# Optimization experiments

Hardware: AMD Instinct MI355X
Metric: run time of the kernel (lower is better)

The kernel has to match this reference:

```python
import jax, jax.numpy as jnp
import numpy as np

B, T, E, H, K = 256, 512, 768, 100, 11
START, STOP = 9, 10
NEG = -1000.0


def setup_inputs() -> dict:
    key = jax.random.key(0)
    ks = jax.random.split(key, 12)
    s = 0.1
    Hd = H // 2  # per-direction hidden (bidirectional)
    trans = jax.random.normal(ks[9], (K, K), jnp.float32)
    trans = trans.at[:, START].set(NEG).at[STOP, :].set(NEG)
    return {
        "embeddings": jax.random.normal(ks[0], (B, T, E), jnp.float32),
        "input_mask": jnp.ones((B, T), jnp.int32),
        "W_ih_f": jax.random.normal(ks[1], (4 * Hd, E), jnp.float32) * s,
        "W_hh_f": jax.random.normal(ks[2], (4 * Hd, Hd), jnp.float32) * s,
        "b_f": jax.random.normal(ks[3], (4 * Hd,), jnp.float32) * s,
        "W_ih_b": jax.random.normal(ks[4], (4 * Hd, E), jnp.float32) * s,
        "W_hh_b": jax.random.normal(ks[5], (4 * Hd, Hd), jnp.float32) * s,
        "b_b": jax.random.normal(ks[6], (4 * Hd,), jnp.float32) * s,
        "W_out": jax.random.normal(ks[7], (K, H), jnp.float32) * s,
        "b_out": jax.random.normal(ks[8], (K,), jnp.float32) * s,
        "transitions": trans,
    }


def _lstm_dir(x, W_ih, W_hh, b, reverse):
    # x: [B, T, E] -> hidden states [B, T, Hd]; zero initial state.
    Bn = x.shape[0]
    Hd = W_hh.shape[1]

    def step(carry, xt):
        h, c = carry
        g = xt @ W_ih.T + h @ W_hh.T + b  # [B, 4*Hd], torch gate order i,f,g,o
        i, f, gg, o = jnp.split(g, 4, axis=-1)
        c = jax.nn.sigmoid(f) * c + jax.nn.sigmoid(i) * jnp.tanh(gg)
        h = jax.nn.sigmoid(o) * jnp.tanh(c)
        return (h, c), h

    init = (jnp.zeros((Bn, Hd), x.dtype), jnp.zeros((Bn, Hd), x.dtype))
    _, hs = jax.lax.scan(step, init, jnp.swapaxes(x, 0, 1), reverse=reverse)
    return jnp.swapaxes(hs, 0, 1)


def _emissions(embeddings, W_ih_f, W_hh_f, b_f, W_ih_b, W_hh_b, b_b, W_out, b_out):
    h_f = _lstm_dir(embeddings, W_ih_f, W_hh_f, b_f, reverse=False)
    h_b = _lstm_dir(embeddings, W_ih_b, W_hh_b, b_b, reverse=True)
    lstm_out = jnp.concatenate([h_f, h_b], axis=-1)  # [B, T, H]
    return lstm_out @ W_out.T + b_out  # [B, T, K]


def reference(embeddings, input_mask, W_ih_f, W_hh_f, b_f, W_ih_b, W_hh_b, b_b,
              W_out, b_out, transitions):
    logits = _emissions(embeddings, W_ih_f, W_hh_f, b_f, W_ih_b, W_hh_b, b_b,
                        W_out, b_out)  # [B, T, K]
    Bn = logits.shape[0]
    mask = (input_mask > 0)

    alpha0 = jnp.full((Bn, K), NEG, logits.dtype).at[:, START].set(0.0)
    idK = jnp.arange(K, dtype=jnp.int32)

    def step(alpha, inp):
        frame, m = inp  # frame [B,K], m [B] bool
        # smat[b, prev, cur] = alpha[b,prev] + frame[b,cur] + trans[prev,cur]
        smat = alpha[:, :, None] + frame[:, None, :] + transitions[None]
        bp = jnp.argmax(smat, axis=1).astype(jnp.int32)          # [B, K]
        new_alpha = jax.nn.logsumexp(smat, axis=1)               # [B, K]
        alpha = jnp.where(m[:, None], new_alpha, alpha)
        bp = jnp.where(m[:, None], bp, idK[None, :])
        return alpha, bp

    alpha_T, bps = jax.lax.scan(
        step, alpha0,
        (jnp.swapaxes(logits, 0, 1), jnp.swapaxes(mask, 0, 1)))  # bps [T,B,K]

    final = alpha_T + transitions[None, :, STOP]                 # [B, K]
    scores = jax.nn.logsumexp(final, axis=1)                     # [B]
    best = jnp.argmax(final, axis=1).astype(jnp.int32)           # [B]

    bidx = jnp.arange(Bn)

    def back(cur, bp_t):
        prev = bp_t[bidx, cur]
        return prev, prev

    # Original skips backtrace[0]; backtrack over positions 1..T-1.
    _, path_prefix = jax.lax.scan(back, best, bps[1:], reverse=True)  # [T-1, B]
    paths = jnp.concatenate(
        [jnp.swapaxes(path_prefix, 0, 1), best[:, None]], axis=1)     # [B, T]
    return scores, paths
```

## Files before the change

### kernel.cpp

```cpp
#include <hip/hip_runtime.h>
#include <math.h>


typedef _Float16 half8 __attribute__((ext_vector_type(8)));
typedef _Float16 half4 __attribute__((ext_vector_type(4)));
typedef float f32x4 __attribute__((ext_vector_type(4)));

__global__ __launch_bounds__(256) void k_gemm_split(
    const float* __restrict__ emb,
    const float* __restrict__ Wf,
    const float* __restrict__ Wb,
    float* __restrict__ xw)
{
    __shared__ _Float16 Ah[128 * 64];
    __shared__ _Float16 Al[128 * 64];
    __shared__ _Float16 Bh[80 * 64];
    __shared__ _Float16 Bl[80 * 64];

    const int bid = blockIdx.x;
    const int wg  = (bid & 7) * 640 + (bid >> 3);
    const int mt  = wg / 5;
    const int nb  = wg - mt * 5;
    const size_t m0 = (size_t)mt * 128;
    const int n0 = nb * 80;

    const int tid  = threadIdx.x;
    const int lane = tid & 63;
    const int w    = tid >> 6;
    const int grp  = lane >> 4;
    const int r16  = lane & 15;

    f32x4 acc[2][5];
    #pragma unroll
    for (int m = 0; m < 2; ++m)
        #pragma unroll
        for (int n = 0; n < 5; ++n) acc[m][n] = (f32x4){0.f, 0.f, 0.f, 0.f};

    for (int kt = 0; kt < 12; ++kt) {
        const int k0 = kt * 64;
        __syncthreads();

        #pragma unroll
        for (int j = 0; j < 8; ++j) {
            const int flat = j * 256 + tid;
            const int row  = flat >> 4;
            const int q    = flat & 15;
            const float4 v = *(const float4*)(emb + (m0 + row) * 768 + k0 + q * 4);
            half4 hv, lv;
            hv[0] = (_Float16)v.x; lv[0] = (_Float16)(v.x - (float)hv[0]);
            hv[1] = (_Float16)v.y; lv[1] = (_Float16)(v.y - (float)hv[1]);
            hv[2] = (_Float16)v.z; lv[2] = (_Float16)(v.z - (float)hv[2]);
            hv[3] = (_Float16)v.w; lv[3] = (_Float16)(v.w - (float)hv[3]);
            const int s    = (q >> 1) ^ (row & 7);
            const int addr = row * 64 + s * 8 + (q & 1) * 4;
            *(half4*)(Ah + addr) = hv;
            *(half4*)(Al + addr) = lv;
        }
        #pragma unroll
        for (int j = 0; j < 5; ++j) {
            const int flat = j * 256 + tid;
            const int row  = flat >> 4;
            const int q    = flat & 15;
            const int n    = n0 + row;
            const float* src = (n < 200) ? (Wf + (size_t)n * 768)
                                         : (Wb + (size_t)(n - 200) * 768);
            const float4 v = *(const float4*)(src + k0 + q * 4);
            half4 hv, lv;
            hv[0] = (_Float16)v.x; lv[0] = (_Float16)(v.x - (float)hv[0]);
            hv[1] = (_Float16)v.y; lv[1] = (_Float16)(v.y - (float)hv[1]);
            hv[2] = (_Float16)v.z; lv[2] = (_Float16)(v.z - (float)hv[2]);
            hv[3] = (_Float16)v.w; lv[3] = (_Float16)(v.w - (float)hv[3]);
            const int s    = (q >> 1) ^ (row & 7);
            const int addr = row * 64 + s * 8 + (q & 1) * 4;
            *(half4*)(Bh + addr) = hv;
            *(half4*)(Bl + addr) = lv;
        }
        __syncthreads();

        #pragma unroll
        for (int ks = 0; ks < 2; ++ks) {
            const int kslot = ks * 4 + grp;
            half8 ah[2], al[2], bh[5], bl[5];
            #pragma unroll
            for (int m = 0; m < 2; ++m) {
                const int row = w * 32 + m * 16 + r16;
                const int ad  = row * 64 + (kslot ^ (row & 7)) * 8;
                ah[m] = *(half8*)(Ah + ad);
                al[m] = *(half8*)(Al + ad);
            }
            #pragma unroll
            for (int n = 0; n < 5; ++n) {
                const int row = n * 16 + r16;
                const int ad  = row * 64 + (kslot ^ (row & 7)) * 8;
                bh[n] = *(half8*)(Bh + ad);
                bl[n] = *(half8*)(Bl + ad);
            }
            #pragma unroll
            for (int m = 0; m < 2; ++m)
                #pragma unroll
                for (int n = 0; n < 5; ++n) {
                    acc[m][n] = __builtin_amdgcn_mfma_f32_16x16x32_f16(ah[m], bh[n], acc[m][n], 0, 0, 0);
                    acc[m][n] = __builtin_amdgcn_mfma_f32_16x16x32_f16(ah[m], bl[n], acc[m][n], 0, 0, 0);
                    acc[m][n] = __builtin_amdgcn_mfma_f32_16x16x32_f16(al[m], bh[n], acc[m][n], 0, 0, 0);
                }
        }
    }

    #pragma unroll
    for (int m = 0; m < 2; ++m) {
        #pragma unroll
        for (int n = 0; n < 5; ++n) {
            #pragma unroll
            for (int i = 0; i < 4; ++i) {
                const size_t row = m0 + w * 32 + m * 16 + (lane >> 4) * 4 + i;
                const int    col = n0 + n * 16 + (lane & 15);
                xw[row * 400 + col] = acc[m][n][i];
            }
        }
    }
}

__global__ __launch_bounds__(256) void k_lstm(
    const float* __restrict__ xw,
    const float* __restrict__ Whh_f,
    const float* __restrict__ Whh_b,
    const float* __restrict__ bf_,
    const float* __restrict__ bb_,
    float* __restrict__ hout)
{
    const int b   = blockIdx.x >> 1;
    const int dir = blockIdx.x & 1;
    const int g   = threadIdx.x;

    __shared__ float h_s[52];
    __shared__ float g_s[200];

    const float* Whh  = dir ? Whh_b : Whh_f;
    const float* bias = dir ? bb_ : bf_;

    float w[52];
    float bg = 0.f;
    if (g < 200) {
        #pragma unroll
        for (int j = 0; j < 50; ++j) w[j] = Whh[g * 50 + j];
        w[50] = 0.f; w[51] = 0.f;
        bg = bias[g];
    } else {
        #pragma unroll
        for (int j = 0; j < 52; ++j) w[j] = 0.f;
    }

    if (g < 52) h_s[g] = 0.f;
    float c = 0.f;
    __syncthreads();

    const size_t base = (size_t)b * 512;

    float xv = 0.f;
    {
        int t0 = dir ? 511 : 0;
        if (g < 200) xv = xw[(base + t0) * 400 + dir * 200 + g];
    }

    for (int it = 0; it < 512; ++it) {
        const int t = dir ? (511 - it) : it;
        float xcur = xv;
        if (it + 1 < 512) {
            int tn = dir ? (510 - it) : (it + 1);
            if (g < 200) xv = xw[(base + tn) * 400 + dir * 200 + g];
        }

        float sum = bg + xcur;
        const float4* h4 = (const float4*)h_s;
        #pragma unroll
        for (int q = 0; q < 13; ++q) {
            float4 hv = h4[q];
            sum = fmaf(w[q * 4 + 0], hv.x, sum);
            sum = fmaf(w[q * 4 + 1], hv.y, sum);
            sum = fmaf(w[q * 4 + 2], hv.z, sum);
            sum = fmaf(w[q * 4 + 3], hv.w, sum);
        }
        if (g < 200) g_s[g] = sum;
        __syncthreads();

        if (g < 50) {
            float gi = g_s[g];
            float gf = g_s[g + 50];
            float gg = g_s[g + 100];
            float go = g_s[g + 150];
            float si = 1.f / (1.f + expf(-gi));
            float sf = 1.f / (1.f + expf(-gf));
            float so = 1.f / (1.f + expf(-go));
            c = sf * c + si * tanhf(gg);
            float h = so * tanhf(c);
            hout[(base + t) * 100 + dir * 50 + g] = h;
            h_s[g] = h;
        }
        __syncthreads();
    }
}

__global__ __launch_bounds__(256) void k_emis(
    const float* __restrict__ hout,
    const float* __restrict__ Wout,
    const float* __restrict__ bout,
    float* __restrict__ logits)
{
    __shared__ float Wl[1104];
    __shared__ float bl[11];
    const int tid = threadIdx.x;
    for (int i = tid; i < 1100; i += 256) Wl[i] = Wout[i];
    if (tid < 11) bl[tid] = bout[tid];
    __syncthreads();

    const size_t bt = (size_t)blockIdx.x * 256 + tid;
    const float4* h4 = (const float4*)(hout + bt * 100);
    float acc[11];
    #pragma unroll
    for (int k = 0; k < 11; ++k) acc[k] = bl[k];
    #pragma unroll
    for (int q = 0; q < 25; ++q) {
        float4 v = h4[q];
        #pragma unroll
        for (int k = 0; k < 11; ++k) {
            const float4 wv = *(const float4*)&Wl[k * 100 + q * 4];
            acc[k] = fmaf(v.x, wv.x, fmaf(v.y, wv.y, fmaf(v.z, wv.z, fmaf(v.w, wv.w, acc[k]))));
        }
    }
    #pragma unroll
    for (int k = 0; k < 11; ++k) logits[bt * 11 + k] = acc[k];
}

__global__ __launch_bounds__(64, 1) void k_crf(
    const float* __restrict__ logits,
    const int* __restrict__ mask,
    const float* __restrict__ trans,
    float* __restrict__ scores,
    float* __restrict__ paths)
{
    const int b = blockIdx.x;
    const int lane = threadIdx.x;

    __shared__ float smat[11 * 12];
    __shared__ float emat[11 * 12];
    __shared__ unsigned char bp[512][12];

    const int  pA = lane / 11, cA = lane - pA * 11;
    const bool hasB = (lane < 57);
    const int  iB = hasB ? (lane + 64) : 0;
    const int  pB = iB / 11, cB = iB - pB * 11;

    const float trA = trans[pA * 11 + cA];
    const float trB = hasB ? trans[pB * 11 + cB] : 0.f;

    float al_c = (lane == 9) ? 0.f : -1000.f;

    const size_t lbase = (size_t)b * 512;

    float fA = logits[lbase * 11 + cA];
    float fB = hasB ? logits[lbase * 11 + cB] : 0.f;
    int   m_cur = mask[lbase];

    for (int t = 0; t < 512; ++t) {
        float fA_n = 0.f, fB_n = 0.f; int m_n = 1;
        if (t + 1 < 512) {
            fA_n = logits[(lbase + t + 1) * 11 + cA];
            if (hasB) fB_n = logits[(lbase + t + 1) * 11 + cB];
            m_n = mask[lbase + t + 1];
        }

        const float alA = __shfl(al_c, pA);
        const float alB = __shfl(al_c, pB);
        const float vvA = (alA + fA) + trA;
        const float vvB = (alB + fB) + trB;
        smat[cA * 12 + pA] = vvA;
        if (hasB) smat[cB * 12 + pB] = vvB;

        float vmax = -1e30f; int amax = 0;
        if (lane < 11) {
            float v[11];
            #pragma unroll
            for (int p = 0; p < 11; ++p) v[p] = smat[lane * 12 + p];
            #pragma unroll
            for (int p = 0; p < 11; ++p) {
                if (v[p] > vmax) { vmax = v[p]; amax = p; }
            }
        }
        const float vmA = __shfl(vmax, cA);
        const float vmB = __shfl(vmax, cB);

        const float eA = expf(vvA - vmA);
        const float eB = expf(vvB - vmB);
        emat[cA * 12 + pA] = eA;
        if (hasB) emat[cB * 12 + pB] = eB;

        if (lane < 11) {
            float e[11];
            #pragma unroll
            for (int p = 0; p < 11; ++p) e[p] = emat[lane * 12 + p];
            float s = 0.f;
            #pragma unroll
            for (int p = 0; p < 11; ++p) s += e[p];
            const float na = vmax + logf(s);
            if (m_cur > 0) {
                al_c = na;
                bp[t][lane] = (unsigned char)amax;
            } else {
                bp[t][lane] = (unsigned char)lane;
            }
        }
        fA = fA_n; fB = fB_n; m_cur = m_n;
    }

    float fin = (lane < 11) ? (al_c + trans[lane * 11 + 10]) : -1e30f;
    float m = fin;
    int am = (lane < 11) ? lane : 1000;
    #pragma unroll
    for (int off = 8; off >= 1; off >>= 1) {
        float om = __shfl_xor(m, off, 16);
        int   oa = __shfl_xor(am, off, 16);
        if (om > m || (om == m && oa < am)) { m = om; am = oa; }
    }
    float s = (lane < 11) ? expf(fin - m) : 0.f;
    #pragma unroll
    for (int off = 8; off >= 1; off >>= 1) s += __shfl_xor(s, off, 16);

    if (lane == 0) {
        scores[b] = m + logf(s);
        int cur = am;
        paths[lbase + 511] = (float)cur;
        for (int t = 511; t >= 1; --t) {
            cur = bp[t][cur];
            paths[lbase + t - 1] = (float)cur;
        }
    }
}

extern "C" void kernel_launch(void* const* d_in, const int* in_sizes, int n_in,
                              void* d_out, int out_size, void* d_ws, size_t ws_size,
                              hipStream_t stream) {
    const float* emb   = (const float*)d_in[0];
    const int*   imask = (const int*)d_in[1];
    const float* Wihf  = (const float*)d_in[2];
    const float* Whhf  = (const float*)d_in[3];
    const float* bf_   = (const float*)d_in[4];
    const float* Wihb  = (const float*)d_in[5];
    const float* Whhb  = (const float*)d_in[6];
    const float* bb_   = (const float*)d_in[7];
    const float* Wout  = (const float*)d_in[8];
    const float* bout  = (const float*)d_in[9];
    const float* trans = (const float*)d_in[10];

    float* out = (float*)d_out;
    float* ws  = (float*)d_ws;
    float* xw     = ws;
    float* hout   = xw + (size_t)131072 * 400;
    float* logits = hout + (size_t)131072 * 100;

    k_gemm_split<<<5120, 256, 0, stream>>>(emb, Wihf, Wihb, xw);
    k_lstm<<<512, 256, 0, stream>>>(xw, Whhf, Whhb, bf_, bb_, hout);
    k_emis<<<512, 256, 0, stream>>>(hout, Wout, bout, logits);
    k_crf<<<256, 64, 0, stream>>>(logits, imask, trans, out, out + 256);
}
```

Before: 1.083 ms.

## Batch 16 sequences per LSTM block and compute recurrence with split-fp16 MFMA

The recurrent LSTM kernel now processes 16 batch chains per block (32 blocks total instead of 512). It computes h@W_hh^T each step with 16x16x32 f16 MFMA, splitting fp32 into hi/lo halves to keep near-fp32 accuracy. Weights are held as MFMA fragments in registers, and the input projection is double-buffered in shared memory. The gate math uses fast exp/rcp intrinsics and only one barrier per step. This targets the per-step latency and the low arithmetic density of one block per sequence. The cost is far fewer blocks on a large GPU, some approximation error from the fast intrinsics and split-fp16, and more shared-memory traffic.

```diff
diff --git a/kernel.cpp b/kernel.cpp
--- a/kernel.cpp
+++ b/kernel.cpp
@@ -120,7 +120,7 @@
     }
 }
 
-__global__ __launch_bounds__(256) void k_lstm(
+__global__ __launch_bounds__(256, 1) void k_lstm(
     const float* __restrict__ xw,
     const float* __restrict__ Whh_f,
     const float* __restrict__ Whh_b,
@@ -128,75 +128,141 @@
     const float* __restrict__ bb_,
     float* __restrict__ hout)
 {
-    const int b   = blockIdx.x >> 1;
-    const int dir = blockIdx.x & 1;
-    const int g   = threadIdx.x;
-
-    __shared__ float h_s[52];
-    __shared__ float g_s[200];
+    const int dir = blockIdx.x >> 4;
+    const int bc  = blockIdx.x & 15;
+    const int tid = threadIdx.x;
+    const int wv  = tid >> 6;
+    const int lane = tid & 63;
+    const int grp  = lane >> 4;
+    const int r16  = lane & 15;
+
+    __shared__ _Float16 Bh[208 * 64];
+    __shared__ _Float16 Bl[208 * 64];
+    __shared__ _Float16 Ahh[16 * 64];
+    __shared__ _Float16 Ahl[16 * 64];
+    __shared__ float g_s[16 * 208];
+    __shared__ float x_s[2][16 * 256];
+    __shared__ float bias_s[208];
 
     const float* Whh  = dir ? Whh_b : Whh_f;
     const float* bias = dir ? bb_ : bf_;
 
-    float w[52];
-    float bg = 0.f;
-    if (g < 200) {
-        #pragma unroll
-        for (int j = 0; j < 50; ++j) w[j] = Whh[g * 50 + j];
-        w[50] = 0.f; w[51] = 0.f;
-        bg = bias[g];
-    } else {
-        #pragma unroll
-        for (int j = 0; j < 52; ++j) w[j] = 0.f;
-    }
-
-    if (g < 52) h_s[g] = 0.f;
-    float c = 0.f;
+    for (int i = tid; i < 208 * 64; i += 256) {
+        const int gate = i >> 6, u = i & 63;
+        const float w = (gate < 200 && u < 50) ? Whh[gate * 50 + u] : 0.f;
+        const _Float16 hi = (_Float16)w;
+        const _Float16 lo = (_Float16)(w - (float)hi);
+        const int ad = gate * 64 + (((u >> 3) ^ (gate & 7)) * 8) + (u & 7);
+        Bh[ad] = hi; Bl[ad] = lo;
+    }
+    for (int i = tid; i < 208; i += 256) bias_s[i] = (i < 200) ? bias[i] : 0.f;
+    for (int i = tid; i < 16 * 64; i += 256) { Ahh[i] = (_Float16)0.f; Ahl[i] = (_Float16)0.f; }
+
+    int ch_[4], un_[4]; bool val_[4];
+    #pragma unroll
+    for (int j = 0; j < 4; ++j) {
+        const int gi = tid + j * 256;
+        val_[j] = (gi < 800);
+        const int gic = val_[j] ? gi : 0;
+        ch_[j] = gic / 50; un_[j] = gic % 50;
+    }
+    float cc[4] = {0.f, 0.f, 0.f, 0.f};
+
+    const size_t bbase = (size_t)(bc * 16) * 512;
+
+    {
+        const int t0 = dir ? 511 : 0;
+        #pragma unroll
+        for (int j = 0; j < 4; ++j) if (val_[j]) {
+            const float4 v = *(const float4*)(xw + (bbase + (size_t)ch_[j] * 512 + t0) * 400 + dir * 200 + un_[j] * 4);
+            *(float4*)(&x_s[0][ch_[j] * 256 + un_[j] * 4]) = v;
+        }
+    }
     __syncthreads();
 
-    const size_t base = (size_t)b * 512;
-
-    float xv = 0.f;
-    {
-        int t0 = dir ? 511 : 0;
-        if (g < 200) xv = xw[(base + t0) * 400 + dir * 200 + g];
-    }
-
+    const int nt0  = (wv == 0) ? 0 : (wv == 1) ? 4 : (wv == 2) ? 7 : 10;
+    const int ncnt = (wv == 0) ? 4 : 3;
+    half8 bhf[4][2], blf[4][2];
+    #pragma unroll
+    for (int j = 0; j < 4; ++j)
+        #pragma unroll
+        for (int ks = 0; ks < 2; ++ks) {
+            const int gate = (nt0 + ((j < ncnt) ? j : 0)) * 16 + r16;
+            const int koct = ks * 4 + grp;
+            const int ad = gate * 64 + ((koct ^ (gate & 7)) * 8);
+            bhf[j][ks] = *(half8*)(Bh + ad);
+            blf[j][ks] = *(half8*)(Bl + ad);
+        }
+
+    int cur = 0;
     for (int it = 0; it < 512; ++it) {
-        const int t = dir ? (511 - it) : it;
-        float xcur = xv;
+        const int t  = dir ? (511 - it) : it;
+        const int tn = dir ? (510 - it) : (it + 1);
+
+        f32x4 acc[4];
+        #pragma unroll
+        for (int j = 0; j < 4; ++j) acc[j] = (f32x4){0.f, 0.f, 0.f, 0.f};
+        #pragma unroll
+        for (int ks = 0; ks < 2; ++ks) {
+            const int koct = ks * 4 + grp;
+            const int aad = r16 * 64 + ((koct ^ (r16 & 7)) * 8);
+            const half8 ah = *(half8*)(Ahh + aad);
+            const half8 al = *(half8*)(Ahl + aad);
+            #pragma unroll
+            for (int j = 0; j < 4; ++j) if (j < ncnt) {
+                acc[j] = __builtin_amdgcn_mfma_f32_16x16x32_f16(ah, bhf[j][ks], acc[j], 0, 0, 0);
+                acc[j] = __builtin_amdgcn_mfma_f32_16x16x32_f16(ah, blf[j][ks], acc[j], 0, 0, 0);
+                acc[j] = __builtin_amdgcn_mfma_f32_16x16x32_f16(al, bhf[j][ks], acc[j], 0, 0, 0);
+            }
+        }
+
+        float4 xf[4];
         if (it + 1 < 512) {
-            int tn = dir ? (510 - it) : (it + 1);
-            if (g < 200) xv = xw[(base + tn) * 400 + dir * 200 + g];
-        }
-
-        float sum = bg + xcur;
-        const float4* h4 = (const float4*)h_s;
-        #pragma unroll
-        for (int q = 0; q < 13; ++q) {
-            float4 hv = h4[q];
-            sum = fmaf(w[q * 4 + 0], hv.x, sum);
-            sum = fmaf(w[q * 4 + 1], hv.y, sum);
-            sum = fmaf(w[q * 4 + 2], hv.z, sum);
-            sum = fmaf(w[q * 4 + 3], hv.w, sum);
-        }
-        if (g < 200) g_s[g] = sum;
+            #pragma unroll
+            for (int j = 0; j < 4; ++j) if (val_[j])
+                xf[j] = *(const float4*)(xw + (bbase + (size_t)ch_[j] * 512 + tn) * 400 + dir * 200 + un_[j] * 4);
+        }
+
+        #pragma unroll
+        for (int j = 0; j < 4; ++j) if (j < ncnt) {
+            const int gate = (nt0 + j) * 16 + r16;
+            #pragma unroll
+            for (int i = 0; i < 4; ++i)
+                g_s[(grp * 4 + i) * 208 + gate] = acc[j][i];
+        }
         __syncthreads();
 
-        if (g < 50) {
-            float gi = g_s[g];
-            float gf = g_s[g + 50];
-            float gg = g_s[g + 100];
-            float go = g_s[g + 150];
-            float si = 1.f / (1.f + expf(-gi));
-            float sf = 1.f / (1.f + expf(-gf));
-            float so = 1.f / (1.f + expf(-go));
-            c = sf * c + si * tanhf(gg);
-            float h = so * tanhf(c);
-            hout[(base + t) * 100 + dir * 50 + g] = h;
-            h_s[g] = h;
-        }
-        __syncthreads();
+        if (it + 1 < 512) {
+            #pragma unroll
+            for (int j = 0; j < 4; ++j) if (val_[j])
+                *(float4*)(&x_s[cur ^ 1][ch_[j] * 256 + un_[j] * 4]) = xf[j];
+        }
+
+        #pragma unroll
+        for (int j = 0; j < 4; ++j) if (val_[j]) {
+            const int chain = ch_[j], u = un_[j];
+            const float* gr = &g_s[chain * 208];
+            const float* xr = &x_s[cur][chain * 256];
+            const float gi_ = (xr[u]       + gr[u])       + bias_s[u];
+            const float gf_ = (xr[50 + u]  + gr[50 + u])  + bias_s[50 + u];
+            const float gg_ = (xr[100 + u] + gr[100 + u]) + bias_s[100 + u];
+            const float go_ = (xr[150 + u] + gr[150 + u]) + bias_s[150 + u];
+            const float si = __builtin_amdgcn_rcpf(1.f + __expf(-gi_));
+            const float sf = __builtin_amdgcn_rcpf(1.f + __expf(-gf_));
+            const float tg = 1.f - 2.f * __builtin_amdgcn_rcpf(__expf(2.f * gg_) + 1.f);
+            cc[j] = sf * cc[j] + si * tg;
+            const float th = 1.f - 2.f * __builtin_amdgcn_rcpf(__expf(2.f * cc[j]) + 1.f);
+            const float so = __builtin_amdgcn_rcpf(1.f + __expf(-go_));
+            const float h = so * th;
+            hout[(bbase + (size_t)chain * 512 + t) * 100 + dir * 50 + u] = h;
+            const _Float16 hhi = (_Float16)h;
+            const _Float16 hlo = (_Float16)(h - (float)hhi);
+            const int aad = chain * 64 + (((u >> 3) ^ (chain & 7)) * 8) + (u & 7);
+            Ahh[aad] = hhi;
+            Ahl[aad] = hlo;
+        }
+        asm volatile("s_waitcnt lgkmcnt(0)\n\ts_barrier" ::: "memory");
+        cur ^= 1;
     }
 }
 
@@ -358,7 +424,7 @@
     float* logits = hout + (size_t)131072 * 100;
 
     k_gemm_split<<<5120, 256, 0, stream>>>(emb, Wihf, Wihb, xw);
-    k_lstm<<<512, 256, 0, stream>>>(xw, Whhf, Whhb, bf_, bb_, hout);
+    k_lstm<<<32, 256, 0, stream>>>(xw, Whhf, Whhb, bf_, bb_, hout);
     k_emis<<<512, 256, 0, stream>>>(hout, Wout, bout, logits);
     k_crf<<<256, 64, 0, stream>>>(logits, imask, trans, out, out + 256);
 }
```

Measured after the change: 2.365 ms. 2.18x slower.

## Restructure LSTM recurrence with LDS weights, double-buffered h, and lightweight barriers

Applied to the files above, without the earlier changes.

Moves the recurrent weight matrix from per-thread registers into transposed shared memory, and double-buffers the hidden state. Each step now uses a custom barrier that waits only on LDS, and four independent FMA chains. Gate activations switch to fast exp/rcp approximations, x-projection loads are prefetched 8 steps ahead, and hidden outputs are buffered and written every 8 steps. The aim is to cut the serial per-step latency of the recurrent loop, at the cost of extra LDS traffic for the weights and slightly less accurate transcendentals.

```diff
diff --git a/kernel.cpp b/kernel.cpp
--- a/kernel.cpp
+++ b/kernel.cpp
@@ -5,6 +5,13 @@
 typedef _Float16 half8 __attribute__((ext_vector_type(8)));
 typedef _Float16 half4 __attribute__((ext_vector_type(4)));
 typedef float f32x4 __attribute__((ext_vector_type(4)));
+
+#define LBAR() do {                                   \
+    __builtin_amdgcn_sched_barrier(0);                \
+    asm volatile("s_waitcnt lgkmcnt(0)");             \
+    __builtin_amdgcn_s_barrier();                     \
+    __builtin_amdgcn_sched_barrier(0);                \
+} while (0)
 
 __global__ __launch_bounds__(256) void k_gemm_split(
     const float* __restrict__ emb,
@@ -132,71 +139,90 @@
     const int dir = blockIdx.x & 1;
     const int g   = threadIdx.x;
 
-    __shared__ float h_s[52];
+    __shared__ __align__(16) float WT4[13][256][4];
+    __shared__ __align__(16) float hb[2][52];
     __shared__ float g_s[200];
 
     const float* Whh  = dir ? Whh_b : Whh_f;
     const float* bias = dir ? bb_ : bf_;
 
-    float w[52];
-    float bg = 0.f;
-    if (g < 200) {
-        #pragma unroll
-        for (int j = 0; j < 50; ++j) w[j] = Whh[g * 50 + j];
-        w[50] = 0.f; w[51] = 0.f;
-        bg = bias[g];
-    } else {
-        #pragma unroll
-        for (int j = 0; j < 52; ++j) w[j] = 0.f;
-    }
-
-    if (g < 52) h_s[g] = 0.f;
+    for (int i = g; i < 13 * 256 * 4; i += 256) ((float*)WT4)[i] = 0.f;
+    __syncthreads();
+    for (int s = g; s < 10000; s += 256) {
+        const int row = s / 50;
+        const int k   = s - row * 50;
+        WT4[k >> 2][row][k & 3] = Whh[s];
+    }
+    const bool gl200 = (g < 200);
+    const bool gl50  = (g < 50);
+    const float bg = gl200 ? bias[g] : 0.f;
+    if (g < 104) ((float*)hb)[g] = 0.f;
     float c = 0.f;
     __syncthreads();
 
     const size_t base = (size_t)b * 512;
-
-    float xv = 0.f;
-    {
-        int t0 = dir ? 511 : 0;
-        if (g < 200) xv = xw[(base + t0) * 400 + dir * 200 + g];
-    }
-
-    for (int it = 0; it < 512; ++it) {
-        const int t = dir ? (511 - it) : it;
-        float xcur = xv;
-        if (it + 1 < 512) {
-            int tn = dir ? (510 - it) : (it + 1);
-            if (g < 200) xv = xw[(base + tn) * 400 + dir * 200 + g];
-        }
-
-        float sum = bg + xcur;
-        const float4* h4 = (const float4*)h_s;
-        #pragma unroll
-        for (int q = 0; q < 13; ++q) {
-            float4 hv = h4[q];
-            sum = fmaf(w[q * 4 + 0], hv.x, sum);
-            sum = fmaf(w[q * 4 + 1], hv.y, sum);
-            sum = fmaf(w[q * 4 + 2], hv.z, sum);
-            sum = fmaf(w[q * 4 + 3], hv.w, sum);
-        }
-        if (g < 200) g_s[g] = sum;
-        __syncthreads();
-
-        if (g < 50) {
-            float gi = g_s[g];
-            float gf = g_s[g + 50];
-            float gg = g_s[g + 100];
-            float go = g_s[g + 150];
-            float si = 1.f / (1.f + expf(-gi));
-            float sf = 1.f / (1.f + expf(-gf));
-            float so = 1.f / (1.f + expf(-go));
-            c = sf * c + si * tanhf(gg);
-            float h = so * tanhf(c);
-            hout[(base + t) * 100 + dir * 50 + g] = h;
-            h_s[g] = h;
-        }
-        __syncthreads();
+    const int col = dir * 200 + (gl200 ? g : 0);
+    const float* wbase = &WT4[0][gl200 ? g : 0][0];
+
+    float xv[8];
+    #pragma unroll
+    for (int k = 0; k < 8; ++k) {
+        const int tt = dir ? (511 - k) : k;
+        xv[k] = gl200 ? xw[(base + tt) * 400 + col] : 0.f;
+    }
+    float hreg[8];
+
+    int cur = 0;
+    for (int it0 = 0; it0 < 512; it0 += 8) {
+        #pragma unroll
+        for (int k = 0; k < 8; ++k) {
+            const int it = it0 + k;
+            const float xcur = xv[k];
+            if (it + 8 < 512) {
+                const int tn = dir ? (511 - (it + 8)) : (it + 8);
+                if (gl200) xv[k] = xw[(base + tn) * 400 + col];
+            }
+
+            const f32x4* h4 = (const f32x4*)(&hb[cur][0]);
+            float s0 = bg + xcur, s1 = 0.f, s2 = 0.f, s3 = 0.f;
+            #pragma unroll
+            for (int q = 0; q < 13; ++q) {
+                const f32x4 wq = *(const f32x4*)(wbase + q * 1024);
+                const f32x4 hv = h4[q];
+                s0 = fmaf(wq[0], hv[0], s0);
+                s1 = fmaf(wq[1], hv[1], s1);
+                s2 = fmaf(wq[2], hv[2], s2);
+                s3 = fmaf(wq[3], hv[3], s3);
+            }
+            const float sum = (s0 + s1) + (s2 + s3);
+            if (gl200) g_s[g] = sum;
+            LBAR();
+
+            if (gl50) {
+                const float gi = g_s[g];
+                const float gf = g_s[g + 50];
+                const float gg = g_s[g + 100];
+                const float go = g_s[g + 150];
+                const float si = __builtin_amdgcn_rcpf(1.f + __expf(-gi));
+                const float sf = __builtin_amdgcn_rcpf(1.f + __expf(-gf));
+                const float tg = 1.f - 2.f * __builtin_amdgcn_rcpf(__expf(2.f * gg) + 1.f);
+                c = sf * c + si * tg;
+                const float th = 1.f - 2.f * __builtin_amdgcn_rcpf(__expf(2.f * c) + 1.f);
+                const float so = __builtin_amdgcn_rcpf(1.f + __expf(-go));
+                const float h = so * th;
+                hreg[k] = h;
+                hb[cur ^ 1][g] = h;
+            }
+            LBAR();
+            cur ^= 1;
+        }
+        if (gl50) {
+            #pragma unroll
+            for (int r = 0; r < 8; ++r) {
+                const int tr_ = dir ? (511 - (it0 + r)) : (it0 + r);
+                hout[(base + tr_) * 100 + dir * 50 + g] = hreg[r];
+            }
+        }
     }
 }
 
```

Result: slower. 1.223 ms (+12.9%).
